# Kernel tuning notes

Measured on AMD Instinct MI355X. Metric: run time of the kernel, lower is better.

The kernel has to match this reference:

```python
import jax, jax.numpy as jnp
import numpy as np

HEAD_SIZE = 64

def setup_inputs() -> dict:
    key = jax.random.key(0)
    k1, k2, k3, k4 = jax.random.split(key, 4)
    B, T, C = 4, 4096, 768
    s = 1.0 / np.sqrt(C)
    return {
        "x": jax.random.normal(k1, (B, T, C), dtype=jnp.float32),
        "Wq": jax.random.normal(k2, (C, HEAD_SIZE), dtype=jnp.float32) * s,
        "Wk": jax.random.normal(k3, (C, HEAD_SIZE), dtype=jnp.float32) * s,
        "Wv": jax.random.normal(k4, (C, HEAD_SIZE), dtype=jnp.float32) * s,
    }

def reference(x, Wq, Wk, Wv):
    # x: [B,T,C]; Wq/Wk/Wv: [C,H]
    T = x.shape[1]
    q = jnp.einsum('btc,ch->bth', x, Wq)
    k = jnp.einsum('btc,ch->bth', x, Wk)
    v = jnp.einsum('btc,ch->bth', x, Wv)
    scale = HEAD_SIZE ** (-0.5)
    wei = jnp.einsum('bth,bsh->bts', q, k) * scale  # [B,T,T]
    causal = jnp.tril(jnp.ones((T, T), dtype=bool))
    wei = jnp.where(causal, wei, -jnp.inf)
    wei = jax.nn.softmax(wei, axis=-1)
    # dropout p=0.0 -> identity
    out = jnp.einsum('bts,bsh->bth', wei, v)  # [B,T,H]
    return out
```

## Files before the change

kernel.cpp:

```cpp
#include <hip/hip_runtime.h>
#include <hip/hip_bf16.h>
#include <stdint.h>

typedef unsigned short u16;
typedef __attribute__((ext_vector_type(8))) __bf16 bf16x8;
typedef __attribute__((ext_vector_type(4))) float f32x4;

#define LOG2E 1.44269504088896340736f
#define FIXED_M 16.0f

__device__ inline u16 f2bf(float f){
  uint32_t u = __float_as_uint(f);
  u += 0x7FFFu + ((u >> 16) & 1u);
  return (u16)(u >> 16);
}
__device__ inline float bf2f(u16 v){
  return __uint_as_float(((uint32_t)v) << 16);
}

__global__ __launch_bounds__(256) void wt_kernel(const float* __restrict__ Wq,
                                                 const float* __restrict__ Wk,
                                                 const float* __restrict__ Wv,
                                                 u16* __restrict__ wtf){
  int idx = blockIdx.x * 256 + threadIdx.x;
  if (idx >= 192 * 768) return;
  int n = idx / 768, c = idx - n * 768;
  int h = n & 63;
  const float* W = (n < 64) ? Wq : ((n < 128) ? Wk : Wv);
  float v = W[c * 64 + h];
  if (n < 64) v *= 0.125f * LOG2E;
  int f = n >> 4, n16 = n & 15;
  int kstep = c >> 5, quad = (c >> 3) & 3, j = c & 7;
  wtf[(size_t)((f * 24 + kstep) * 64 + quad * 16 + n16) * 8 + j] = f2bf(v);
}

__global__ __launch_bounds__(256) void proj_kernel(const float* __restrict__ x,
                                                   const u16* __restrict__ wtf,
                                                   u16* __restrict__ qs,
                                                   u16* __restrict__ ksf,
                                                   u16* __restrict__ vtf){
  __shared__ u16 At[2 * 24 * 64 * 8];
  const int tid = threadIdx.x;
  const int w = tid >> 6, lane = tid & 63;
  const int n16 = lane & 15, quad = lane >> 4;
  const int rt = blockIdx.x * 32;

  const float* xb = x + (size_t)rt * 768;
  for (int p = 0; p < 3; ++p){
    float4 t[8];
#pragma unroll
    for (int i = 0; i < 8; ++i)
      t[i] = *(const float4*)(xb + (size_t)((p * 8 + i) * 256 + tid) * 4);
#pragma unroll
    for (int i = 0; i < 8; ++i){
      int l = (p * 8 + i) * 256 + tid;
      int row = l / 192, c4 = l - row * 192;
      int g = row >> 4, r16 = row & 15;
      int ksn = c4 >> 3, qd = (c4 >> 1) & 3, j0 = (c4 & 1) * 4;
      int idx = (((g * 24 + ksn) * 64 + qd * 16 + r16) * 8 + j0) ^ ((ksn & 7) << 3);
      union { ushort4 s; u16 e[4]; } pk;
      pk.e[0] = f2bf(t[i].x); pk.e[1] = f2bf(t[i].y);
      pk.e[2] = f2bf(t[i].z); pk.e[3] = f2bf(t[i].w);
      *(ushort4*)&At[idx] = pk.s;
    }
  }
  __syncthreads();

  const f32x4 fz = {0.f, 0.f, 0.f, 0.f};
  f32x4 acc[2][3];
#pragma unroll
  for (int g = 0; g < 2; ++g)
#pragma unroll
    for (int j = 0; j < 3; ++j) acc[g][j] = fz;

#pragma unroll
  for (int kst = 0; kst < 24; ++kst){
    const int sw = (kst & 7) << 3;
    bf16x8 a0 = *(const bf16x8*)&At[(((0 * 24 + kst) * 64 + lane) * 8) ^ sw];
    bf16x8 a1 = *(const bf16x8*)&At[(((1 * 24 + kst) * 64 + lane) * 8) ^ sw];
#pragma unroll
    for (int j = 0; j < 3; ++j){
      bf16x8 bfr = *(const bf16x8*)(wtf + (size_t)(((3 * w + j) * 24 + kst) * 64 + lane) * 8);
      acc[0][j] = __builtin_amdgcn_mfma_f32_16x16x32_bf16(a0, bfr, acc[0][j], 0, 0, 0);
      acc[1][j] = __builtin_amdgcn_mfma_f32_16x16x32_bf16(a1, bfr, acc[1][j], 0, 0, 0);
    }
  }
  __syncthreads();

#pragma unroll
  for (int j = 0; j < 3; ++j){
    const int F = 3 * w + j;
    const int s = F >> 2, c0 = (F & 3) * 16;
#pragma unroll
    for (int g = 0; g < 2; ++g){
#pragma unroll
      for (int r = 0; r < 4; ++r){
        u16 val = f2bf(acc[g][j][r]);
        int row = g * 16 + quad * 4 + r;
        if (s < 2) At[s * 2304 + row * 72 + c0 + n16] = val;
        else       At[4608 + (c0 + n16) * 40 + row]   = val;
      }
    }
  }
  __syncthreads();

  const int bb = rt >> 12, t0 = rt & 4095;
  const int kt = t0 >> 6, f0 = (rt >> 4) & 3, half0 = (rt >> 5) & 1;
  {
    int row = tid >> 3, hc = tid & 7;
    uint4 qv = *(const uint4*)&At[row * 72 + hc * 8];
    *(uint4*)(qs + (size_t)(rt + row) * 64 + hc * 8) = qv;
  }
  {
    int fi = tid >> 7, half = (tid >> 6) & 1, l2 = tid & 63;
    int nn = l2 & 15, qq = l2 >> 4;
    uint4 kv = *(const uint4*)&At[2304 + (fi * 16 + nn) * 72 + half * 32 + qq * 8];
    size_t off = ((((size_t)(bb * 64 + kt) * 4 + f0 + fi) * 2 + half) * 64 + l2) * 8;
    *(uint4*)(ksf + off) = kv;
  }
  {
    int f = tid >> 6, l2 = tid & 63;
    int nn = l2 & 15, qq = l2 >> 4;
    uint4 vv = *(const uint4*)&At[4608 + (f * 16 + nn) * 40 + qq * 8];
    size_t off = ((((size_t)(bb * 64 + kt) * 4 + f) * 2 + half0) * 64 + l2) * 8;
    *(uint4*)(vtf + off) = vv;
  }
}

__global__ __launch_bounds__(256) void flash_part(const u16* __restrict__ qs,
                                                  const u16* __restrict__ ksf,
                                                  const u16* __restrict__ vtf,
                                                  u16* __restrict__ Opart,
                                                  float* __restrict__ ml){
  const int b  = blockIdx.x >> 9;
  const int qt = (blockIdx.x >> 3) & 63;
  const int ck = blockIdx.x & 7;
  const int kt0 = ck * 8;
  if (kt0 > qt) return;
  const int kt1 = min(qt, kt0 + 7);

  __shared__ u16 Ps[4 * 16 * 72];
  const int tid = threadIdx.x;
  const int w = tid >> 6, lane = tid & 63;
  const int n16 = lane & 15, quad = lane >> 4;

  const u16* qb = qs + (size_t)b * 262144;
  const u16* kp = ksf + (size_t)b * 262144 + (size_t)kt0 * 4096 + lane * 8;
  const u16* vp = vtf + (size_t)b * 262144 + (size_t)kt0 * 4096 + lane * 8;

  const int qrow = qt * 64 + w * 16 + n16;
  bf16x8 qA0 = *(const bf16x8*)(qb + (size_t)qrow * 64 + quad * 8);
  bf16x8 qA1 = *(const bf16x8*)(qb + (size_t)qrow * 64 + 32 + quad * 8);

  const f32x4 fz = {0.f, 0.f, 0.f, 0.f};
  f32x4 O[4];
  float rs[4] = {0.f, 0.f, 0.f, 0.f};
#pragma unroll
  for (int f = 0; f < 4; ++f) O[f] = fz;

  bf16x8 kf[8];
#pragma unroll
  for (int i = 0; i < 8; ++i) kf[i] = *(const bf16x8*)(kp + i * 512);

  for (int kt = kt0; kt <= kt1; ++kt){
    bf16x8 vf[8];
#pragma unroll
    for (int i = 0; i < 8; ++i)
      vf[i] = *(const bf16x8*)(vp + (size_t)(kt - kt0) * 4096 + i * 512);

    f32x4 S[4];
#pragma unroll
    for (int f = 0; f < 4; ++f){
      f32x4 s = fz;
      s = __builtin_amdgcn_mfma_f32_16x16x32_bf16(qA0, kf[f * 2],     s, 0, 0, 0);
      s = __builtin_amdgcn_mfma_f32_16x16x32_bf16(qA1, kf[f * 2 + 1], s, 0, 0, 0);
      S[f] = s;
    }

    if (kt < kt1){
#pragma unroll
      for (int i = 0; i < 8; ++i)
        kf[i] = *(const bf16x8*)(kp + (size_t)(kt - kt0 + 1) * 4096 + i * 512);
    }

    if (kt == qt){
#pragma unroll
      for (int f = 0; f < 4; ++f){
#pragma unroll
        for (int r = 0; r < 4; ++r){
          int col = kt * 64 + f * 16 + n16;
          int row = qt * 64 + w * 16 + quad * 4 + r;
          if (col > row) S[f][r] = -1e30f;
        }
      }
    }

#pragma unroll
    for (int f = 0; f < 4; ++f){
#pragma unroll
      for (int r = 0; r < 4; ++r){
        float p = __builtin_amdgcn_exp2f(S[f][r] - FIXED_M);
        S[f][r] = p;
        rs[r] += p;
      }
    }

#pragma unroll
    for (int f = 0; f < 4; ++f){
#pragma unroll
      for (int r = 0; r < 4; ++r)
        Ps[(w * 16 + quad * 4 + r) * 72 + f * 16 + n16] = f2bf(S[f][r]);
    }
    bf16x8 pA0 = *(const bf16x8*)&Ps[(w * 16 + n16) * 72 + quad * 8];
    bf16x8 pA1 = *(const bf16x8*)&Ps[(w * 16 + n16) * 72 + 32 + quad * 8];

#pragma unroll
    for (int f = 0; f < 4; ++f){
      O[f] = __builtin_amdgcn_mfma_f32_16x16x32_bf16(pA0, vf[f * 2],     O[f], 0, 0, 0);
      O[f] = __builtin_amdgcn_mfma_f32_16x16x32_bf16(pA1, vf[f * 2 + 1], O[f], 0, 0, 0);
    }
  }

#pragma unroll
  for (int r = 0; r < 4; ++r){
#pragma unroll
    for (int off = 1; off < 16; off <<= 1)
      rs[r] += __shfl_xor(rs[r], off, 16);
  }

  const size_t oidx = (size_t)blockIdx.x * 4096;
#pragma unroll
  for (int f = 0; f < 4; ++f){
#pragma unroll
    for (int r = 0; r < 4; ++r){
      int row_local = w * 16 + quad * 4 + r;
      Opart[oidx + (size_t)row_local * 64 + f * 16 + n16] = f2bf(O[f][r]);
    }
  }
  if (n16 == 0){
    float* lp = ml + (size_t)blockIdx.x * 64;
#pragma unroll
    for (int r = 0; r < 4; ++r)
      lp[w * 16 + quad * 4 + r] = rs[r];
  }
}

__global__ __launch_bounds__(256) void combine_kernel(const u16* __restrict__ Opart,
                                                      const float* __restrict__ ml,
                                                      float* __restrict__ out){
  const int gid = blockIdx.x * 256 + threadIdx.x;
  const size_t base = (size_t)gid * 4;
  const int bq = gid >> 10;
  const int rem = (int)(base & 4095);
  const int row = rem >> 6;
  const int qt = bq & 63;
  const int nc = (qt >> 3) + 1;

  float L = 0.f;
  float a0 = 0.f, a1 = 0.f, a2 = 0.f, a3 = 0.f;
  for (int c = 0; c < nc; ++c){
    L += ml[((size_t)bq * 8 + c) * 64 + row];
    const u16* p = Opart + ((size_t)bq * 8 + c) * 4096 + rem;
    uint2 d = *(const uint2*)p;
    a0 += bf2f((u16)(d.x & 0xffffu));
    a1 += bf2f((u16)(d.x >> 16));
    a2 += bf2f((u16)(d.y & 0xffffu));
    a3 += bf2f((u16)(d.y >> 16));
  }
  const float invL = 1.0f / L;
  float4 v = {a0 * invL, a1 * invL, a2 * invL, a3 * invL};
  *(float4*)(out + base) = v;
}

extern "C" void kernel_launch(void* const* d_in, const int* in_sizes, int n_in,
                              void* d_out, int out_size, void* d_ws, size_t ws_size,
                              hipStream_t stream){
  const float* x  = (const float*)d_in[0];
  const float* Wq = (const float*)d_in[1];
  const float* Wk = (const float*)d_in[2];
  const float* Wv = (const float*)d_in[3];
  float* out = (float*)d_out;

  u16* qs  = (u16*)d_ws;
  u16* ksf = qs  + (size_t)16384 * 64;
  u16* vtf = ksf + (size_t)16384 * 64;
  u16* wtf = vtf + (size_t)16384 * 64;
  u16* Opart = wtf + (size_t)192 * 768;
  float* ml = (float*)(Opart + (size_t)2048 * 4096);

  wt_kernel<<<576, 256, 0, stream>>>(Wq, Wk, Wv, wtf);
  proj_kernel<<<512, 256, 0, stream>>>(x, wtf, qs, ksf, vtf);
  flash_part<<<2048, 256, 0, stream>>>(qs, ksf, vtf, Opart, ml);
  combine_kernel<<<1024, 256, 0, stream>>>(Opart, ml, out);
}
```

Measured before the change: 142.6 us.

## Use 128-row query tiles with 4-tile KV chunks in split-K flash attention

Each flash block now handles 128 query rows, with two 16-row MFMA subtiles per wave, and KV chunks of 4 tiles instead of 8. Each K/V fragment loaded from global memory is reused across twice as many query rows, which halves KV load traffic per unit of work. The combine kernel and workspace layout are updated to the new block indexing. The cost is more register pressure (doubled O/S accumulators) and more partial outputs written to and read from the workspace.

Result: no change. 142.3 us (-0.2%).

```diff
diff --git a/kernel.cpp b/kernel.cpp
--- a/kernel.cpp
+++ b/kernel.cpp
@@ -133,13 +133,14 @@
                                                   u16* __restrict__ Opart,
                                                   float* __restrict__ ml){
   const int b  = blockIdx.x >> 9;
-  const int qt = (blockIdx.x >> 3) & 63;
-  const int ck = blockIdx.x & 7;
-  const int kt0 = ck * 8;
-  if (kt0 > qt) return;
-  const int kt1 = min(qt, kt0 + 7);
-
-  __shared__ u16 Ps[4 * 16 * 72];
+  const int qt = (blockIdx.x >> 4) & 31;
+  const int ck = blockIdx.x & 15;
+  const int kt0 = ck * 4;
+  const int ktmax = 2 * qt + 1;
+  if (kt0 > ktmax) return;
+  const int kt1 = min(ktmax, kt0 + 3);
+
+  __shared__ u16 Ps[128 * 72];
   const int tid = threadIdx.x;
   const int w = tid >> 6, lane = tid & 63;
   const int n16 = lane & 15, quad = lane >> 4;
@@ -148,15 +149,21 @@
   const u16* kp = ksf + (size_t)b * 262144 + (size_t)kt0 * 4096 + lane * 8;
   const u16* vp = vtf + (size_t)b * 262144 + (size_t)kt0 * 4096 + lane * 8;
 
-  const int qrow = qt * 64 + w * 16 + n16;
-  bf16x8 qA0 = *(const bf16x8*)(qb + (size_t)qrow * 64 + quad * 8);
-  bf16x8 qA1 = *(const bf16x8*)(qb + (size_t)qrow * 64 + 32 + quad * 8);
+  bf16x8 qA[2][2];
+#pragma unroll
+  for (int m = 0; m < 2; ++m){
+    const size_t qrow = (size_t)(qt * 128 + w * 32 + m * 16 + n16) * 64;
+    qA[m][0] = *(const bf16x8*)(qb + qrow + quad * 8);
+    qA[m][1] = *(const bf16x8*)(qb + qrow + 32 + quad * 8);
+  }
 
   const f32x4 fz = {0.f, 0.f, 0.f, 0.f};
-  f32x4 O[4];
-  float rs[4] = {0.f, 0.f, 0.f, 0.f};
-#pragma unroll
-  for (int f = 0; f < 4; ++f) O[f] = fz;
+  f32x4 O[2][4];
+  float rs[2][4];
+#pragma unroll
+  for (int m = 0; m < 2; ++m)
+#pragma unroll
+    for (int f = 0; f < 4; ++f){ O[m][f] = fz; rs[m][f] = 0.f; }
 
   bf16x8 kf[8];
 #pragma unroll
@@ -168,14 +175,16 @@
     for (int i = 0; i < 8; ++i)
       vf[i] = *(const bf16x8*)(vp + (size_t)(kt - kt0) * 4096 + i * 512);
 
-    f32x4 S[4];
-#pragma unroll
-    for (int f = 0; f < 4; ++f){
-      f32x4 s = fz;
-      s = __builtin_amdgcn_mfma_f32_16x16x32_bf16(qA0, kf[f * 2],     s, 0, 0, 0);
-      s = __builtin_amdgcn_mfma_f32_16x16x32_bf16(qA1, kf[f * 2 + 1], s, 0, 0, 0);
-      S[f] = s;
-    }
+    f32x4 S[2][4];
+#pragma unroll
+    for (int m = 0; m < 2; ++m)
+#pragma unroll
+      for (int f = 0; f < 4; ++f){
+        f32x4 s = fz;
+        s = __builtin_amdgcn_mfma_f32_16x16x32_bf16(qA[m][0], kf[f * 2],     s, 0, 0, 0);
+        s = __builtin_amdgcn_mfma_f32_16x16x32_bf16(qA[m][1], kf[f * 2 + 1], s, 0, 0, 0);
+        S[m][f] = s;
+      }
 
     if (kt < kt1){
 #pragma unroll
@@ -183,65 +192,82 @@
         kf[i] = *(const bf16x8*)(kp + (size_t)(kt - kt0 + 1) * 4096 + i * 512);
     }
 
-    if (kt == qt){
+    if (kt >= 2 * qt){
+#pragma unroll
+      for (int m = 0; m < 2; ++m)
+#pragma unroll
+        for (int f = 0; f < 4; ++f)
+#pragma unroll
+          for (int r = 0; r < 4; ++r){
+            int col = kt * 64 + f * 16 + n16;
+            int row = qt * 128 + w * 32 + m * 16 + quad * 4 + r;
+            if (col > row) S[m][f][r] = -1e30f;
+          }
+    }
+
+#pragma unroll
+    for (int m = 0; m < 2; ++m)
+#pragma unroll
+      for (int f = 0; f < 4; ++f)
+#pragma unroll
+        for (int r = 0; r < 4; ++r){
+          float p = __builtin_amdgcn_exp2f(S[m][f][r] - FIXED_M);
+          S[m][f][r] = p;
+          rs[m][r] += p;
+        }
+
+#pragma unroll
+    for (int m = 0; m < 2; ++m)
 #pragma unroll
       for (int f = 0; f < 4; ++f){
-#pragma unroll
-        for (int r = 0; r < 4; ++r){
-          int col = kt * 64 + f * 16 + n16;
-          int row = qt * 64 + w * 16 + quad * 4 + r;
-          if (col > row) S[f][r] = -1e30f;
-        }
-      }
-    }
-
-#pragma unroll
-    for (int f = 0; f < 4; ++f){
+        u16* p = &Ps[(w * 32 + m * 16 + quad * 4) * 72 + f * 16 + n16];
+        p[0]   = f2bf(S[m][f][0]);
+        p[72]  = f2bf(S[m][f][1]);
+        p[144] = f2bf(S[m][f][2]);
+        p[216] = f2bf(S[m][f][3]);
+      }
+    bf16x8 pA[2][2];
+#pragma unroll
+    for (int m = 0; m < 2; ++m){
+      pA[m][0] = *(const bf16x8*)&Ps[(w * 32 + m * 16 + n16) * 72 + quad * 8];
+      pA[m][1] = *(const bf16x8*)&Ps[(w * 32 + m * 16 + n16) * 72 + 32 + quad * 8];
+    }
+
+#pragma unroll
+    for (int m = 0; m < 2; ++m)
+#pragma unroll
+      for (int f = 0; f < 4; ++f){
+        O[m][f] = __builtin_amdgcn_mfma_f32_16x16x32_bf16(pA[m][0], vf[f * 2],     O[m][f], 0, 0, 0);
+        O[m][f] = __builtin_amdgcn_mfma_f32_16x16x32_bf16(pA[m][1], vf[f * 2 + 1], O[m][f], 0, 0, 0);
+      }
+  }
+
+#pragma unroll
+  for (int m = 0; m < 2; ++m)
+#pragma unroll
+    for (int r = 0; r < 4; ++r){
+#pragma unroll
+      for (int off = 1; off < 16; off <<= 1)
+        rs[m][r] += __shfl_xor(rs[m][r], off, 16);
+    }
+
+  const size_t oidx = (size_t)blockIdx.x * 8192;
+#pragma unroll
+  for (int m = 0; m < 2; ++m)
+#pragma unroll
+    for (int f = 0; f < 4; ++f)
 #pragma unroll
       for (int r = 0; r < 4; ++r){
-        float p = __builtin_amdgcn_exp2f(S[f][r] - FIXED_M);
-        S[f][r] = p;
-        rs[r] += p;
-      }
-    }
-
-#pragma unroll
-    for (int f = 0; f < 4; ++f){
+        int row_local = w * 32 + m * 16 + quad * 4 + r;
+        Opart[oidx + (size_t)row_local * 64 + f * 16 + n16] = f2bf(O[m][f][r]);
+      }
+  if (n16 == 0){
+    float* lp = ml + (size_t)blockIdx.x * 128;
+#pragma unroll
+    for (int m = 0; m < 2; ++m)
 #pragma unroll
       for (int r = 0; r < 4; ++r)
-        Ps[(w * 16 + quad * 4 + r) * 72 + f * 16 + n16] = f2bf(S[f][r]);
-    }
-    bf16x8 pA0 = *(const bf16x8*)&Ps[(w * 16 + n16) * 72 + quad * 8];
-    bf16x8 pA1 = *(const bf16x8*)&Ps[(w * 16 + n16) * 72 + 32 + quad * 8];
-
-#pragma unroll
-    for (int f = 0; f < 4; ++f){
-      O[f] = __builtin_amdgcn_mfma_f32_16x16x32_bf16(pA0, vf[f * 2],     O[f], 0, 0, 0);
-      O[f] = __builtin_amdgcn_mfma_f32_16x16x32_bf16(pA1, vf[f * 2 + 1], O[f], 0, 0, 0);
-    }
-  }
-
-#pragma unroll
-  for (int r = 0; r < 4; ++r){
-#pragma unroll
-    for (int off = 1; off < 16; off <<= 1)
-      rs[r] += __shfl_xor(rs[r], off, 16);
-  }
-
-  const size_t oidx = (size_t)blockIdx.x * 4096;
-#pragma unroll
-  for (int f = 0; f < 4; ++f){
-#pragma unroll
-    for (int r = 0; r < 4; ++r){
-      int row_local = w * 16 + quad * 4 + r;
-      Opart[oidx + (size_t)row_local * 64 + f * 16 + n16] = f2bf(O[f][r]);
-    }
-  }
-  if (n16 == 0){
-    float* lp = ml + (size_t)blockIdx.x * 64;
-#pragma unroll
-    for (int r = 0; r < 4; ++r)
-      lp[w * 16 + quad * 4 + r] = rs[r];
+        lp[w * 32 + m * 16 + quad * 4 + r] = rs[m][r];
   }
 }
 
@@ -249,18 +275,17 @@
                                                       const float* __restrict__ ml,
                                                       float* __restrict__ out){
   const int gid = blockIdx.x * 256 + threadIdx.x;
-  const size_t base = (size_t)gid * 4;
-  const int bq = gid >> 10;
-  const int rem = (int)(base & 4095);
+  const int bq = gid >> 11;
+  const int rem = (gid & 2047) * 4;
   const int row = rem >> 6;
-  const int qt = bq & 63;
-  const int nc = (qt >> 3) + 1;
+  const int qt = bq & 31;
+  const int nc = (2 * qt + 5) >> 2;
 
   float L = 0.f;
   float a0 = 0.f, a1 = 0.f, a2 = 0.f, a3 = 0.f;
   for (int c = 0; c < nc; ++c){
-    L += ml[((size_t)bq * 8 + c) * 64 + row];
-    const u16* p = Opart + ((size_t)bq * 8 + c) * 4096 + rem;
+    L += ml[((size_t)bq * 16 + c) * 128 + row];
+    const u16* p = Opart + ((size_t)bq * 16 + c) * 8192 + rem;
     uint2 d = *(const uint2*)p;
     a0 += bf2f((u16)(d.x & 0xffffu));
     a1 += bf2f((u16)(d.x >> 16));
@@ -269,7 +294,7 @@
   }
   const float invL = 1.0f / L;
   float4 v = {a0 * invL, a1 * invL, a2 * invL, a3 * invL};
-  *(float4*)(out + base) = v;
+  *(float4*)(out + (size_t)gid * 4) = v;
 }
 
 extern "C" void kernel_launch(void* const* d_in, const int* in_sizes, int n_in,
@@ -286,7 +311,7 @@
   u16* vtf = ksf + (size_t)16384 * 64;
   u16* wtf = vtf + (size_t)16384 * 64;
   u16* Opart = wtf + (size_t)192 * 768;
-  float* ml = (float*)(Opart + (size_t)2048 * 4096);
+  float* ml = (float*)(Opart + (size_t)2048 * 8192);
 
   wt_kernel<<<576, 256, 0, stream>>>(Wq, Wk, Wv, wtf);
   proj_kernel<<<512, 256, 0, stream>>>(x, wtf, qs, ksf, vtf);
```
